# Performance work log

Hardware: AMD Instinct MI355X
Metric: run time of the kernel (lower is better)

## Reference

```python
import jax, jax.numpy as jnp
import numpy as np

NPOINT = 1024
K = 16
D_MODEL = 512
EPS = 1e-5


def _fps(xyz, npoint):
    # deterministic farthest point sampling (start at index 0)
    B, N, _ = xyz.shape
    def step(carry, _):
        dist, far = carry                                   # [B,N], [B]
        cent = jnp.take_along_axis(xyz, far[:, None, None], axis=1)  # [B,1,3]
        d = jnp.sum((xyz - cent) ** 2, axis=-1)             # [B,N]
        dist = jnp.minimum(dist, d)
        nxt = jnp.argmax(dist, axis=-1).astype(jnp.int32)
        return (dist, nxt), far
    init = (jnp.full((B, N), 1e10, xyz.dtype), jnp.zeros((B,), jnp.int32))
    _, idx = jax.lax.scan(step, init, None, length=npoint)
    return jnp.transpose(idx)                                # [B, npoint]


def _bn_relu(x, gamma, beta):
    # BatchNorm (training-mode batch stats, biased var) over all axes but channel-last
    axes = tuple(range(x.ndim - 1))
    mu = jnp.mean(x, axes, keepdims=True)
    var = jnp.var(x, axes, keepdims=True)
    return jax.nn.relu((x - mu) * jax.lax.rsqrt(var + EPS) * gamma + beta)


def _forward(xyz, feat, w1, b1, g1, bt1, fc1_w, fc1_b, wq, wk, wv, fc2_w, fc2_b,
             w2, b2, g2, bt2):
    B, N, C = feat.shape
    fps_idx = _fps(xyz, NPOINT)                              # [B,S]
    new_xyz = jnp.take_along_axis(xyz, fps_idx[:, :, None], axis=1)  # [B,S,3]
    # kNN of sampled centers against all points: squared distances [B,S,N]
    d = (jnp.sum(new_xyz ** 2, -1)[:, :, None]
         + jnp.sum(xyz ** 2, -1)[:, None, :]
         - 2.0 * jnp.einsum('bsc,bnc->bsn', new_xyz, xyz))
    _, knn_idx = jax.lax.top_k(-d, K)                        # [B,S,K]
    grouped = jnp.take_along_axis(
        feat, knn_idx.reshape(B, -1)[:, :, None], axis=1
    ).reshape(B, NPOINT, K, C)                               # [B,S,K,C]
    # mlp1: 1x1 conv + BN + ReLU (channel-last)
    x = _bn_relu(grouped @ w1.T + b1, g1, bt1)
    # TransformerBlock: local self-attention over the K neighbors
    pre = x
    h = x @ fc1_w.T + fc1_b                                  # [B,S,K,D]
    q, kk, v = h @ wq.T, h @ wk.T, h @ wv.T
    attn = jax.nn.softmax(
        jnp.einsum('bsnd,bsmd->bsnm', q, kk) / np.sqrt(D_MODEL), axis=-1)
    res = jnp.einsum('bsnm,bsmd->bsnd', attn, v)
    x = res @ fc2_w.T + fc2_b + pre                          # [B,S,K,C]
    # mlp2: 1x1 conv + BN + ReLU -> out_channel
    x = _bn_relu(x @ w2.T + b2, g2, bt2)                     # [B,S,K,out]
    new_feat = jnp.max(x, axis=2)                            # max-pool over neighbors
    return new_xyz, new_feat


def setup_inputs() -> dict:
    key = jax.random.key(0)
    ks = jax.random.split(key, 12)
    s = 0.02
    return {
        'xyz': jax.random.uniform(ks[0], (8, 4096, 3), jnp.float32),
        'feat': jax.random.normal(ks[1], (8, 4096, 64), jnp.float32),
        'w1': jax.random.normal(ks[2], (64, 64), jnp.float32) * s,
        'b1': jnp.zeros((64,), jnp.float32),
        'g1': jnp.ones((64,), jnp.float32),
        'bt1': jnp.zeros((64,), jnp.float32),
        'fc1_w': jax.random.normal(ks[3], (512, 64), jnp.float32) * s,
        'fc1_b': jnp.zeros((512,), jnp.float32),
        'wq': jax.random.normal(ks[4], (512, 512), jnp.float32) * s,
        'wk': jax.random.normal(ks[5], (512, 512), jnp.float32) * s,
        'wv': jax.random.normal(ks[6], (512, 512), jnp.float32) * s,
        'fc2_w': jax.random.normal(ks[7], (64, 512), jnp.float32) * s,
        'fc2_b': jnp.zeros((64,), jnp.float32),
        'w2': jax.random.normal(ks[8], (128, 64), jnp.float32) * s,
        'b2': jnp.zeros((128,), jnp.float32),
        'g2': jnp.ones((128,), jnp.float32),
        'bt2': jnp.zeros((128,), jnp.float32),
    }


def reference(xyz, feat, w1, b1, g1, bt1, fc1_w, fc1_b, wq, wk, wv, fc2_w, fc2_b,
              w2, b2, g2, bt2):
    return _forward(xyz, feat, w1, b1, g1, bt1, fc1_w, fc1_b, wq, wk, wv,
                    fc2_w, fc2_b, w2, b2, g2, bt2)
```

## Files before the change

kernel.cpp:

```cpp
#include <hip/hip_runtime.h>

#define EPSBN 1e-5f
#define INVSQ 0.04419417382415922f

#define WS_KNN_IDX   32768u
#define WS_X1        1048576u
#define WS_BNP1      34603008u
#define WS_BN1S      34865152u
#define WS_BNP2      34865664u
#define WS_BN2S      35914240u
#define WS_A         35915264u
#define WS_B         36046336u
#define WS_QB        36177408u
#define WS_KB        36179456u
#define WS_WC        36181504u
#define WS_G         36312576u
#define WS_ZT        36328960u
#define WS_U         36345344u
#define WS_W         36345600u
#define WS_TB        36345856u
#define WS_CC        36346112u
#define WS_PTS4      36346368u

__global__ __launch_bounds__(256) void prep1_kernel(const float* __restrict__ wq,
                                                    const float* __restrict__ wk,
                                                    const float* __restrict__ fc1w,
                                                    const float* __restrict__ fc1b,
                                                    const float* __restrict__ fc2w,
                                                    const float* __restrict__ wv,
                                                    const float* __restrict__ xyz,
                                                    float* __restrict__ A, float* __restrict__ B,
                                                    float* __restrict__ qb, float* __restrict__ kb,
                                                    float* __restrict__ Wc,
                                                    float4* __restrict__ pts4) {
  const int blk = blockIdx.x;
  if (blk < 256) {
    int id = blk * 256 + threadIdx.x;
    int which = id >> 15;
    int rem = id & 32767;
    int r = rem >> 6, i = rem & 63;
    const float* W = which ? wk : wq;
    float s = 0.f;
    for (int d = 0; d < 512; ++d) s = fmaf(W[r * 512 + d], fc1w[d * 64 + i], s);
    (which ? B : A)[r * 64 + i] = s;
    if (i == 0) {
      float sb = 0.f;
      for (int d = 0; d < 512; ++d) sb = fmaf(W[r * 512 + d], fc1b[d], sb);
      (which ? kb : qb)[r] = sb;
    }
  } else if (blk < 384) {
    int id = (blk - 256) * 256 + threadIdx.x;
    int c = id >> 9, d = id & 511;
    float s = 0.f;
    for (int e = 0; e < 512; ++e) s = fmaf(fc2w[c * 512 + e], wv[e * 512 + d], s);
    Wc[c * 512 + d] = s;
  } else {
    int id = (blk - 384) * 256 + threadIdx.x;
    float x = xyz[id * 3 + 0], y = xyz[id * 3 + 1], z = xyz[id * 3 + 2];
    float pp = __fadd_rn(__fadd_rn(__fmul_rn(x, x), __fmul_rn(y, y)), __fmul_rn(z, z));
    pts4[id] = make_float4(x, y, z, pp);
  }
}

__global__ __launch_bounds__(256) void prep2_kernel(const float* __restrict__ A,
                                                    const float* __restrict__ B,
                                                    const float* __restrict__ qb,
                                                    const float* __restrict__ kb,
                                                    const float* __restrict__ Wc,
                                                    const float* __restrict__ fc1w,
                                                    const float* __restrict__ fc1b,
                                                    const float* __restrict__ fc2b,
                                                    float* __restrict__ G, float* __restrict__ u,
                                                    float* __restrict__ w, float* __restrict__ cc,
                                                    float* __restrict__ ZT, float* __restrict__ tb) {
  const int blk = blockIdx.x;
  if (blk < 17) {
    int id = blk * 256 + threadIdx.x;
    if (id < 4096) {
      int i = id >> 6, j = id & 63;
      float s = 0.f;
      for (int d = 0; d < 512; ++d) s = fmaf(A[d * 64 + i], B[d * 64 + j], s);
      G[i * 64 + j] = s * INVSQ;
    } else if (id < 4160) {
      int i = id - 4096; float s = 0.f;
      for (int d = 0; d < 512; ++d) s = fmaf(A[d * 64 + i], kb[d], s);
      u[i] = s * INVSQ;
    } else if (id < 4224) {
      int j = id - 4160; float s = 0.f;
      for (int d = 0; d < 512; ++d) s = fmaf(B[d * 64 + j], qb[d], s);
      w[j] = s * INVSQ;
    } else if (id == 4224) {
      float s = 0.f;
      for (int d = 0; d < 512; ++d) s = fmaf(qb[d], kb[d], s);
      cc[0] = s * INVSQ;
    }
  } else {
    int id = (blk - 17) * 256 + threadIdx.x;
    if (id < 4096) {
      int i = id >> 6, c = id & 63;
      float s = 0.f;
      for (int d = 0; d < 512; ++d) s = fmaf(Wc[c * 512 + d], fc1w[d * 64 + i], s);
      ZT[i * 64 + c] = s;
    } else if (id < 4160) {
      int c = id - 4096; float s = 0.f;
      for (int d = 0; d < 512; ++d) s = fmaf(Wc[c * 512 + d], fc1b[d], s);
      tb[c] = s + fc2b[c];
    }
  }
}

#define FPS_REDSTEP(CTRL)                                                              \
  {                                                                                    \
    unsigned lo2 = (unsigned)__builtin_amdgcn_update_dpp(0, (int)klo, CTRL, 0xF, 0xF, true); \
    unsigned hi2 = (unsigned)__builtin_amdgcn_update_dpp(0, (int)khi, CTRL, 0xF, 0xF, true); \
    bool tk = (hi2 > khi) || (hi2 == khi && lo2 > klo);                                \
    khi = tk ? hi2 : khi; klo = tk ? lo2 : klo;                                        \
  }

__global__ __launch_bounds__(256) void fps_kernel(const float4* __restrict__ pts4,
                                                  float* __restrict__ out_xyz) {
  __shared__ float4 spts[4096];
  __shared__ float4 cent4[1024];
  __shared__ unsigned long long red[2][4];
  const int b = blockIdx.x;
  const int t = threadIdx.x;
  const int lane = t & 63, wid = t >> 6;
  const float4* pb = pts4 + (size_t)b * 4096;
  float px[16], py[16], pz[16], pd[16];
#pragma unroll
  for (int i = 0; i < 16; ++i) {
    int j = i * 256 + t;
    float4 p = pb[j];
    spts[j] = p;
    px[i] = p.x; py[i] = p.y; pz[i] = p.z; pd[i] = 1e10f;
  }
  __syncthreads();
  float4 c4 = spts[0];
  for (int it = 0; it < 1024; ++it) {
    if (t == 0) cent4[it] = c4;
    float bv = -1.0f; int bj = 0;
#pragma unroll
    for (int i = 0; i < 16; ++i) {
      float dx = __fsub_rn(px[i], c4.x);
      float dy = __fsub_rn(py[i], c4.y);
      float dz = __fsub_rn(pz[i], c4.z);
      float d = __fadd_rn(__fadd_rn(__fmul_rn(dx, dx), __fmul_rn(dy, dy)), __fmul_rn(dz, dz));
      float nd = fminf(pd[i], d);
      pd[i] = nd;
      bool g = nd > bv;
      bv = g ? nd : bv;
      bj = g ? (i * 256 + t) : bj;
    }
    unsigned klo = 4095u - (unsigned)bj;
    unsigned khi = __float_as_uint(bv);
    FPS_REDSTEP(0x111)
    FPS_REDSTEP(0x112)
    FPS_REDSTEP(0x114)
    FPS_REDSTEP(0x118)
    FPS_REDSTEP(0x142)
    FPS_REDSTEP(0x143)
    unsigned wlo = (unsigned)__builtin_amdgcn_readlane((int)klo, 63);
    unsigned whi = (unsigned)__builtin_amdgcn_readlane((int)khi, 63);
    const int par = it & 1;
    if (lane == 0) red[par][wid] = (((unsigned long long)whi) << 32) | wlo;
    __syncthreads();
    const ulonglong2* r2 = reinterpret_cast<const ulonglong2*>(&red[par][0]);
    ulonglong2 ka = r2[0];
    ulonglong2 kb = r2[1];
    unsigned long long m0 = (ka.x > ka.y) ? ka.x : ka.y;
    unsigned long long m1 = (kb.x > kb.y) ? kb.x : kb.y;
    unsigned long long k0 = (m0 > m1) ? m0 : m1;
    int jw = 4095 - (int)(unsigned)(k0 & 0xFFFFFFFFull);
    c4 = spts[jw];
  }
  __syncthreads();
  for (int o = t; o < 3072; o += 256) {
    int j = o / 3;
    int c = o - 3 * j;
    out_xyz[(size_t)b * 3072 + o] = (&cent4[j].x)[c];
  }
}

__global__ __launch_bounds__(256) void knn_kernel(const float4* __restrict__ pts4,
                                                  const float* __restrict__ new_xyz,
                                                  int* __restrict__ knn_idx) {
  const int t = threadIdx.x & 63;
  const int wave = (blockIdx.x << 2) | (threadIdx.x >> 6);
  const int b = wave >> 10;
  const float4* P = pts4 + (size_t)b * 4096;
  const float cx = new_xyz[(size_t)wave * 3 + 0];
  const float cy = new_xyz[(size_t)wave * 3 + 1];
  const float cz = new_xyz[(size_t)wave * 3 + 2];
  const float cc = __fadd_rn(__fadd_rn(__fmul_rn(cx, cx), __fmul_rn(cy, cy)), __fmul_rn(cz, cz));
  float ldd[16]; int ldi[16];
#pragma unroll
  for (int q = 0; q < 16; ++q) { ldd[q] = 3.4e38f; ldi[q] = 0x7fffffff; }
  for (int i = 0; i < 64; ++i) {
    int j = i * 64 + t;
    float4 p = P[j];
    float dot = __fadd_rn(__fadd_rn(__fmul_rn(cx, p.x), __fmul_rn(cy, p.y)), __fmul_rn(cz, p.z));
    float d = __fsub_rn(__fadd_rn(cc, p.w), __fmul_rn(2.0f, dot));
    if (d < ldd[15] || (d == ldd[15] && j < ldi[15])) {
      float cd = d; int ci = j;
#pragma unroll
      for (int q = 0; q < 16; ++q) {
        bool sw = (cd < ldd[q]) || (cd == ldd[q] && ci < ldi[q]);
        float td = ldd[q]; int ti = ldi[q];
        if (sw) { ldd[q] = cd; ldi[q] = ci; cd = td; ci = ti; }
      }
    }
  }
  float cd = ldd[0]; int ci = ldi[0];
  int* op = knn_idx + (size_t)wave * 16;
#pragma unroll 1
  for (int k = 0; k < 16; ++k) {
    float wd = cd; int wi = ci;
#pragma unroll
    for (int off = 1; off < 64; off <<= 1) {
      float ov = __shfl_xor(wd, off);
      int   oi = __shfl_xor(wi, off);
      bool tk = (ov < wd) || (ov == wd && oi < wi);
      wd = tk ? ov : wd; wi = tk ? oi : wi;
    }
    if (t == 0) op[k] = wi;
    if (wd == cd && wi == ci) {
#pragma unroll
      for (int q = 0; q < 15; ++q) { ldd[q] = ldd[q + 1]; ldi[q] = ldi[q + 1]; }
      ldd[15] = 3.4e38f; ldi[15] = 0x7fffffff;
    }
    cd = ldd[0]; ci = ldi[0];
  }
}

__global__ __launch_bounds__(256) void mlp1_kernel(const float* __restrict__ feat,
                                                   const int* __restrict__ knn_idx,
                                                   const float* __restrict__ w1,
                                                   const float* __restrict__ b1,
                                                   float* __restrict__ x1) {
  __shared__ float w1s[64 * 64];
  __shared__ float b1s[64];
  const int t = threadIdx.x;
  for (int i = t; i < 4096; i += 256) w1s[i] = w1[i];
  if (t < 64) b1s[t] = b1[t];
  __syncthreads();
  const int pos = blockIdx.x * 256 + t;
  const int b = pos >> 14;
  const int n = knn_idx[pos];
  const float4* fp = reinterpret_cast<const float4*>(feat + ((size_t)(b * 4096 + n)) * 64);
  float4 fr[16];
#pragma unroll
  for (int i = 0; i < 16; ++i) fr[i] = fp[i];
  float4* op = reinterpret_cast<float4*>(x1 + (size_t)pos * 64);
#pragma unroll
  for (int cq = 0; cq < 16; ++cq) {
    float a0 = b1s[cq * 4 + 0], a1 = b1s[cq * 4 + 1], a2 = b1s[cq * 4 + 2], a3 = b1s[cq * 4 + 3];
#pragma unroll
    for (int iq = 0; iq < 16; ++iq) {
      float4 f4 = fr[iq];
      float4 wa = *reinterpret_cast<const float4*>(&w1s[(cq * 4 + 0) * 64 + iq * 4]);
      float4 wb = *reinterpret_cast<const float4*>(&w1s[(cq * 4 + 1) * 64 + iq * 4]);
      float4 wc = *reinterpret_cast<const float4*>(&w1s[(cq * 4 + 2) * 64 + iq * 4]);
      float4 wd = *reinterpret_cast<const float4*>(&w1s[(cq * 4 + 3) * 64 + iq * 4]);
      a0 += f4.x * wa.x + f4.y * wa.y + f4.z * wa.z + f4.w * wa.w;
      a1 += f4.x * wb.x + f4.y * wb.y + f4.z * wb.z + f4.w * wb.w;
      a2 += f4.x * wc.x + f4.y * wc.y + f4.z * wc.z + f4.w * wc.w;
      a3 += f4.x * wd.x + f4.y * wd.y + f4.z * wd.z + f4.w * wd.w;
    }
    op[cq] = make_float4(a0, a1, a2, a3);
  }
}

__global__ __launch_bounds__(256) void bn1_stats_kernel(const float* __restrict__ x1,
                                                        float* __restrict__ bnp1) {
  __shared__ float ls[4][64], lq[4][64];
  const int t = threadIdx.x, c = t & 63, g = t >> 6;
  const float* p = x1 + ((size_t)blockIdx.x * 256 + g * 64) * 64 + c;
  float s = 0.f, s2 = 0.f;
  for (int i = 0; i < 64; ++i) { float v = p[(size_t)i * 64]; s += v; s2 = fmaf(v, v, s2); }
  ls[g][c] = s; lq[g][c] = s2;
  __syncthreads();
  if (t < 64) {
    bnp1[blockIdx.x * 128 + t]      = ls[0][t] + ls[1][t] + ls[2][t] + ls[3][t];
    bnp1[blockIdx.x * 128 + 64 + t] = lq[0][t] + lq[1][t] + lq[2][t] + lq[3][t];
  }
}

__global__ __launch_bounds__(256) void bn1_final_kernel(const float* __restrict__ bnp1,
                                                        const float* __restrict__ g1,
                                                        const float* __restrict__ bt1,
                                                        float* __restrict__ bn1s) {
  __shared__ float rs[4][64], rq[4][64];
  const int t = threadIdx.x, c = t & 63, g = t >> 6;
  float S = 0.f, Q = 0.f;
  for (int i = g * 128; i < g * 128 + 128; ++i) {
    S += bnp1[i * 128 + c];
    Q += bnp1[i * 128 + 64 + c];
  }
  rs[g][c] = S; rq[g][c] = Q;
  __syncthreads();
  if (t < 64) {
    float Sa = rs[0][t] + rs[1][t] + rs[2][t] + rs[3][t];
    float Qa = rq[0][t] + rq[1][t] + rq[2][t] + rq[3][t];
    float m = Sa * (1.0f / 131072.0f);
    float var = Qa * (1.0f / 131072.0f) - m * m;
    float sc = g1[t] * rsqrtf(var + EPSBN);
    bn1s[t] = sc;
    bn1s[64 + t] = bt1[t] - m * sc;
  }
}

__global__ __launch_bounds__(64) void transformer_fused(
    float* __restrict__ x1, const float* __restrict__ bn1s,
    const float* __restrict__ G, const float* __restrict__ u, const float* __restrict__ w,
    const float* __restrict__ cc, const float* __restrict__ ZT, const float* __restrict__ tb) {
  __shared__ float pre[16][65];
  __shared__ float ts[16][65];
  __shared__ float ys[16][65];
  __shared__ float ss[16][17];
  __shared__ float spu[16], spw[16];
  const int c = threadIdx.x;
  const size_t base = (size_t)blockIdx.x * 1024;
  const float sc = bn1s[c], sh = bn1s[64 + c];
  float pc[16];
#pragma unroll
  for (int k = 0; k < 16; ++k) {
    float v = x1[base + k * 64 + c];
    float p = fmaxf(0.f, v * sc + sh);
    pc[k] = p; pre[k][c] = p;
  }
  __syncthreads();
  float tcol[16], ycol[16];
#pragma unroll
  for (int k = 0; k < 16; ++k) { tcol[k] = 0.f; ycol[k] = 0.f; }
  for (int i = 0; i < 64; ++i) {
    float g = G[i * 64 + c];
    float z = ZT[i * 64 + c];
#pragma unroll
    for (int k = 0; k < 16; ++k) {
      float p = pre[k][i];
      tcol[k] = fmaf(p, g, tcol[k]);
      ycol[k] = fmaf(p, z, ycol[k]);
    }
  }
#pragma unroll
  for (int k = 0; k < 16; ++k) { ts[k][c] = tcol[k]; ys[k][c] = ycol[k]; }
  if (c < 16) {
    float s = 0.f;
    for (int i = 0; i < 64; ++i) s = fmaf(pre[c][i], u[i], s);
    spu[c] = s;
  } else if (c < 32) {
    int m = c - 16; float s = 0.f;
    for (int i = 0; i < 64; ++i) s = fmaf(pre[m][i], w[i], s);
    spw[m] = s;
  }
  __syncthreads();
  {
    const float cval = cc[0];
    const int m = c & 15, nb = c >> 4;
#pragma unroll
    for (int ng = 0; ng < 4; ++ng) {
      int n = ng * 4 + nb;
      float s = 0.f;
      for (int i = 0; i < 64; ++i) s = fmaf(ts[n][i], pre[m][i], s);
      ss[n][m] = s + spu[n] + spw[m] + cval;
    }
  }
  __syncthreads();
  if (c < 16) {
    float mx = -3.4e38f;
#pragma unroll
    for (int m = 0; m < 16; ++m) mx = fmaxf(mx, ss[c][m]);
    float e[16], sum = 0.f;
#pragma unroll
    for (int m = 0; m < 16; ++m) { e[m] = expf(ss[c][m] - mx); sum += e[m]; }
    float r = 1.0f / sum;
#pragma unroll
    for (int m = 0; m < 16; ++m) ss[c][m] = e[m] * r;
  }
  __syncthreads();
  const float tbc = tb[c];
  float o[16];
#pragma unroll
  for (int k = 0; k < 16; ++k) o[k] = 0.f;
#pragma unroll
  for (int m = 0; m < 16; ++m) {
    float yv = ys[m][c];
#pragma unroll
    for (int k = 0; k < 16; ++k) o[k] = fmaf(ss[k][m], yv, o[k]);
  }
#pragma unroll
  for (int k = 0; k < 16; ++k) x1[base + k * 64 + c] = o[k] + tbc + pc[k];
}

__global__ __launch_bounds__(256) void bn2_stats_kernel(const float* __restrict__ x2,
                                                        const float* __restrict__ w2,
                                                        const float* __restrict__ b2,
                                                        float* __restrict__ bnp2) {
  __shared__ float sx2[128 * 64];
  __shared__ float ps[2][128], pq[2][128];
  const int t = threadIdx.x;
  const float4* s4 = reinterpret_cast<const float4*>(x2 + (size_t)blockIdx.x * 128 * 64);
  float4* d4 = reinterpret_cast<float4*>(sx2);
  for (int i = 0; i < 8; ++i) d4[i * 256 + t] = s4[i * 256 + t];
  __syncthreads();
  const int c = t & 127, h = t >> 7;
  float4 wreg[16];
  const float4* w4 = reinterpret_cast<const float4*>(w2 + c * 64);
#pragma unroll
  for (int i = 0; i < 16; ++i) wreg[i] = w4[i];
  const float bb = b2[c];
  float s = 0.f, q = 0.f;
  for (int p = 0; p < 64; ++p) {
    const float4* xr = reinterpret_cast<const float4*>(&sx2[(h * 64 + p) * 64]);
    float acc = bb;
#pragma unroll
    for (int i = 0; i < 16; ++i) {
      float4 xv = xr[i];
      acc += xv.x * wreg[i].x + xv.y * wreg[i].y + xv.z * wreg[i].z + xv.w * wreg[i].w;
    }
    s += acc; q = fmaf(acc, acc, q);
  }
  ps[h][c] = s; pq[h][c] = q;
  __syncthreads();
  if (t < 128) {
    bnp2[blockIdx.x * 256 + t]       = ps[0][t] + ps[1][t];
    bnp2[blockIdx.x * 256 + 128 + t] = pq[0][t] + pq[1][t];
  }
}

__global__ __launch_bounds__(512) void bn2_final_kernel(const float* __restrict__ bnp2,
                                                        const float* __restrict__ g2,
                                                        const float* __restrict__ bt2,
                                                        float* __restrict__ bn2s) {
  __shared__ float rs[4][128], rq[4][128];
  const int t = threadIdx.x, c = t & 127, g = t >> 7;
  float S = 0.f, Q = 0.f;
  for (int i = g * 256; i < g * 256 + 256; ++i) {
    S += bnp2[i * 256 + c];
    Q += bnp2[i * 256 + 128 + c];
  }
  rs[g][c] = S; rq[g][c] = Q;
  __syncthreads();
  if (t < 128) {
    float Sa = rs[0][t] + rs[1][t] + rs[2][t] + rs[3][t];
    float Qa = rq[0][t] + rq[1][t] + rq[2][t] + rq[3][t];
    float m = Sa * (1.0f / 131072.0f);
    float var = Qa * (1.0f / 131072.0f) - m * m;
    float sc = g2[t] * rsqrtf(var + EPSBN);
    bn2s[t] = sc;
    bn2s[128 + t] = bt2[t] - m * sc;
  }
}

__global__ __launch_bounds__(128) void final_kernel(const float* __restrict__ x2,
                                                    const float* __restrict__ w2,
                                                    const float* __restrict__ b2,
                                                    const float* __restrict__ bn2s,
                                                    float* __restrict__ out) {
  __shared__ float sx2[16 * 64];
  const int t = threadIdx.x;
  const float4* s4 = reinterpret_cast<const float4*>(x2 + (size_t)blockIdx.x * 1024);
  float4* d4 = reinterpret_cast<float4*>(sx2);
  for (int i = 0; i < 2; ++i) d4[i * 128 + t] = s4[i * 128 + t];
  __syncthreads();
  const int c = t;
  float4 wreg[16];
  const float4* w4 = reinterpret_cast<const float4*>(w2 + c * 64);
#pragma unroll
  for (int i = 0; i < 16; ++i) wreg[i] = w4[i];
  const float bb = b2[c], sc = bn2s[c], sh = bn2s[128 + c];
  float mx = -3.4e38f;
  for (int k = 0; k < 16; ++k) {
    const float4* xr = reinterpret_cast<const float4*>(&sx2[k * 64]);
    float acc = bb;
#pragma unroll
    for (int i = 0; i < 16; ++i) {
      float4 xv = xr[i];
      acc += xv.x * wreg[i].x + xv.y * wreg[i].y + xv.z * wreg[i].z + xv.w * wreg[i].w;
    }
    float y = fmaxf(0.f, acc * sc + sh);
    mx = fmaxf(mx, y);
  }
  out[24576 + (size_t)blockIdx.x * 128 + c] = mx;
}

extern "C" void kernel_launch(void* const* d_in, const int* in_sizes, int n_in,
                              void* d_out, int out_size, void* d_ws, size_t ws_size,
                              hipStream_t stream) {
  const float* xyz  = (const float*)d_in[0];
  const float* feat = (const float*)d_in[1];
  const float* w1   = (const float*)d_in[2];
  const float* b1   = (const float*)d_in[3];
  const float* g1   = (const float*)d_in[4];
  const float* bt1  = (const float*)d_in[5];
  const float* fc1w = (const float*)d_in[6];
  const float* fc1b = (const float*)d_in[7];
  const float* wq   = (const float*)d_in[8];
  const float* wk   = (const float*)d_in[9];
  const float* wv   = (const float*)d_in[10];
  const float* fc2w = (const float*)d_in[11];
  const float* fc2b = (const float*)d_in[12];
  const float* w2   = (const float*)d_in[13];
  const float* b2   = (const float*)d_in[14];
  const float* g2   = (const float*)d_in[15];
  const float* bt2  = (const float*)d_in[16];
  float* out = (float*)d_out;
  char* ws = (char*)d_ws;

  int*    knn_idx = (int*)(ws + WS_KNN_IDX);
  float*  x1      = (float*)(ws + WS_X1);
  float*  bnp1    = (float*)(ws + WS_BNP1);
  float*  bn1s    = (float*)(ws + WS_BN1S);
  float*  bnp2    = (float*)(ws + WS_BNP2);
  float*  bn2s    = (float*)(ws + WS_BN2S);
  float*  Abuf    = (float*)(ws + WS_A);
  float*  Bbuf    = (float*)(ws + WS_B);
  float*  qb      = (float*)(ws + WS_QB);
  float*  kb      = (float*)(ws + WS_KB);
  float*  Wc      = (float*)(ws + WS_WC);
  float*  G       = (float*)(ws + WS_G);
  float*  ZT      = (float*)(ws + WS_ZT);
  float*  u       = (float*)(ws + WS_U);
  float*  w       = (float*)(ws + WS_W);
  float*  tb      = (float*)(ws + WS_TB);
  float*  cc      = (float*)(ws + WS_CC);
  float4* pts4    = (float4*)(ws + WS_PTS4);

  prep1_kernel<<<512, 256, 0, stream>>>(wq, wk, fc1w, fc1b, fc2w, wv, xyz,
                                        Abuf, Bbuf, qb, kb, Wc, pts4);
  prep2_kernel<<<34, 256, 0, stream>>>(Abuf, Bbuf, qb, kb, Wc, fc1w, fc1b, fc2b,
                                       G, u, w, cc, ZT, tb);

  fps_kernel<<<8, 256, 0, stream>>>(pts4, out);
  knn_kernel<<<2048, 256, 0, stream>>>(pts4, out, knn_idx);
  mlp1_kernel<<<512, 256, 0, stream>>>(feat, knn_idx, w1, b1, x1);
  bn1_stats_kernel<<<512, 256, 0, stream>>>(x1, bnp1);
  bn1_final_kernel<<<1, 256, 0, stream>>>(bnp1, g1, bt1, bn1s);
  transformer_fused<<<8192, 64, 0, stream>>>(x1, bn1s, G, u, w, cc, ZT, tb);
  bn2_stats_kernel<<<1024, 256, 0, stream>>>(x1, w2, b2, bnp2);
  bn2_final_kernel<<<1, 512, 0, stream>>>(bnp2, g2, bt2, bn2s);
  final_kernel<<<8192, 128, 0, stream>>>(x1, w2, b2, bn2s, out);
}
```

Before: 1.323 ms.

## Fuse prep2 into FPS launch, keep FPS centroids in registers, fuse BN1 stats

Merges the prep2 weight-precompute blocks into the FPS launch as extra blocks so they run alongside the 8 long-running FPS blocks. FPS no longer stages all points in shared memory. Each wave extracts its candidate centroid coordinates from registers with readlane and publishes them next to the reduction key, which removes a dependent LDS lookup on the serial per-iteration path. BN1 partial statistics are computed at the end of mlp1 instead of in a separate kernel, dropping a launch, at the cost of an extra block barrier and re-reading x1 from global memory.

```diff
diff --git a/kernel.cpp b/kernel.cpp
--- a/kernel.cpp
+++ b/kernel.cpp
@@ -62,53 +62,6 @@
   }
 }
 
-__global__ __launch_bounds__(256) void prep2_kernel(const float* __restrict__ A,
-                                                    const float* __restrict__ B,
-                                                    const float* __restrict__ qb,
-                                                    const float* __restrict__ kb,
-                                                    const float* __restrict__ Wc,
-                                                    const float* __restrict__ fc1w,
-                                                    const float* __restrict__ fc1b,
-                                                    const float* __restrict__ fc2b,
-                                                    float* __restrict__ G, float* __restrict__ u,
-                                                    float* __restrict__ w, float* __restrict__ cc,
-                                                    float* __restrict__ ZT, float* __restrict__ tb) {
-  const int blk = blockIdx.x;
-  if (blk < 17) {
-    int id = blk * 256 + threadIdx.x;
-    if (id < 4096) {
-      int i = id >> 6, j = id & 63;
-      float s = 0.f;
-      for (int d = 0; d < 512; ++d) s = fmaf(A[d * 64 + i], B[d * 64 + j], s);
-      G[i * 64 + j] = s * INVSQ;
-    } else if (id < 4160) {
-      int i = id - 4096; float s = 0.f;
-      for (int d = 0; d < 512; ++d) s = fmaf(A[d * 64 + i], kb[d], s);
-      u[i] = s * INVSQ;
-    } else if (id < 4224) {
-      int j = id - 4160; float s = 0.f;
-      for (int d = 0; d < 512; ++d) s = fmaf(B[d * 64 + j], qb[d], s);
-      w[j] = s * INVSQ;
-    } else if (id == 4224) {
-      float s = 0.f;
-      for (int d = 0; d < 512; ++d) s = fmaf(qb[d], kb[d], s);
-      cc[0] = s * INVSQ;
-    }
-  } else {
-    int id = (blk - 17) * 256 + threadIdx.x;
-    if (id < 4096) {
-      int i = id >> 6, c = id & 63;
-      float s = 0.f;
-      for (int d = 0; d < 512; ++d) s = fmaf(Wc[c * 512 + d], fc1w[d * 64 + i], s);
-      ZT[i * 64 + c] = s;
-    } else if (id < 4160) {
-      int c = id - 4096; float s = 0.f;
-      for (int d = 0; d < 512; ++d) s = fmaf(Wc[c * 512 + d], fc1b[d], s);
-      tb[c] = s + fc2b[c];
-    }
-  }
-}
-
 #define FPS_REDSTEP(CTRL)                                                              \
   {                                                                                    \
     unsigned lo2 = (unsigned)__builtin_amdgcn_update_dpp(0, (int)klo, CTRL, 0xF, 0xF, true); \
@@ -117,11 +70,54 @@
     khi = tk ? hi2 : khi; klo = tk ? lo2 : klo;                                        \
   }
 
-__global__ __launch_bounds__(256) void fps_kernel(const float4* __restrict__ pts4,
-                                                  float* __restrict__ out_xyz) {
-  __shared__ float4 spts[4096];
+__global__ __launch_bounds__(256) void fps_prep2_kernel(
+    const float4* __restrict__ pts4, float* __restrict__ out_xyz,
+    const float* __restrict__ A, const float* __restrict__ B,
+    const float* __restrict__ qb, const float* __restrict__ kb,
+    const float* __restrict__ Wc, const float* __restrict__ fc1w,
+    const float* __restrict__ fc1b, const float* __restrict__ fc2b,
+    float* __restrict__ G, float* __restrict__ u, float* __restrict__ w,
+    float* __restrict__ cc, float* __restrict__ ZT, float* __restrict__ tb) {
+  if (blockIdx.x >= 8) {
+    const int blk = blockIdx.x - 8;
+    if (blk < 17) {
+      int id = blk * 256 + threadIdx.x;
+      if (id < 4096) {
+        int i = id >> 6, j = id & 63;
+        float s = 0.f;
+        for (int d = 0; d < 512; ++d) s = fmaf(A[d * 64 + i], B[d * 64 + j], s);
+        G[i * 64 + j] = s * INVSQ;
+      } else if (id < 4160) {
+        int i = id - 4096; float s = 0.f;
+        for (int d = 0; d < 512; ++d) s = fmaf(A[d * 64 + i], kb[d], s);
+        u[i] = s * INVSQ;
+      } else if (id < 4224) {
+        int j = id - 4160; float s = 0.f;
+        for (int d = 0; d < 512; ++d) s = fmaf(B[d * 64 + j], qb[d], s);
+        w[j] = s * INVSQ;
+      } else if (id == 4224) {
+        float s = 0.f;
+        for (int d = 0; d < 512; ++d) s = fmaf(qb[d], kb[d], s);
+        cc[0] = s * INVSQ;
+      }
+    } else {
+      int id = (blk - 17) * 256 + threadIdx.x;
+      if (id < 4096) {
+        int i = id >> 6, c = id & 63;
+        float s = 0.f;
+        for (int d = 0; d < 512; ++d) s = fmaf(Wc[c * 512 + d], fc1w[d * 64 + i], s);
+        ZT[i * 64 + c] = s;
+      } else if (id < 4160) {
+        int c = id - 4096; float s = 0.f;
+        for (int d = 0; d < 512; ++d) s = fmaf(Wc[c * 512 + d], fc1b[d], s);
+        tb[c] = s + fc2b[c];
+      }
+    }
+    return;
+  }
   __shared__ float4 cent4[1024];
-  __shared__ unsigned long long red[2][4];
+  __shared__ unsigned long long redk[2][4];
+  __shared__ float4 redc[2][4];
   const int b = blockIdx.x;
   const int t = threadIdx.x;
   const int lane = t & 63, wid = t >> 6;
@@ -129,21 +125,19 @@
   float px[16], py[16], pz[16], pd[16];
 #pragma unroll
   for (int i = 0; i < 16; ++i) {
-    int j = i * 256 + t;
-    float4 p = pb[j];
-    spts[j] = p;
+    float4 p = pb[i * 256 + t];
     px[i] = p.x; py[i] = p.y; pz[i] = p.z; pd[i] = 1e10f;
   }
-  __syncthreads();
-  float4 c4 = spts[0];
+  float4 cini = pb[0];
+  float cx = cini.x, cy = cini.y, cz = cini.z;
   for (int it = 0; it < 1024; ++it) {
-    if (t == 0) cent4[it] = c4;
+    if (t == 0) cent4[it] = make_float4(cx, cy, cz, 0.f);
     float bv = -1.0f; int bj = 0;
 #pragma unroll
     for (int i = 0; i < 16; ++i) {
-      float dx = __fsub_rn(px[i], c4.x);
-      float dy = __fsub_rn(py[i], c4.y);
-      float dz = __fsub_rn(pz[i], c4.z);
+      float dx = __fsub_rn(px[i], cx);
+      float dy = __fsub_rn(py[i], cy);
+      float dz = __fsub_rn(pz[i], cz);
       float d = __fadd_rn(__fadd_rn(__fmul_rn(dx, dx), __fmul_rn(dy, dy)), __fmul_rn(dz, dz));
       float nd = fminf(pd[i], d);
       pd[i] = nd;
@@ -161,17 +155,48 @@
     FPS_REDSTEP(0x143)
     unsigned wlo = (unsigned)__builtin_amdgcn_readlane((int)klo, 63);
     unsigned whi = (unsigned)__builtin_amdgcn_readlane((int)khi, 63);
+    int jw = 4095 - (int)wlo;
+    int ol = jw & 63;
+    int slot = jw >> 8;
+    float ox, oy, oz;
+    switch (slot) {
+      case 0:  ox = px[0];  oy = py[0];  oz = pz[0];  break;
+      case 1:  ox = px[1];  oy = py[1];  oz = pz[1];  break;
+      case 2:  ox = px[2];  oy = py[2];  oz = pz[2];  break;
+      case 3:  ox = px[3];  oy = py[3];  oz = pz[3];  break;
+      case 4:  ox = px[4];  oy = py[4];  oz = pz[4];  break;
+      case 5:  ox = px[5];  oy = py[5];  oz = pz[5];  break;
+      case 6:  ox = px[6];  oy = py[6];  oz = pz[6];  break;
+      case 7:  ox = px[7];  oy = py[7];  oz = pz[7];  break;
+      case 8:  ox = px[8];  oy = py[8];  oz = pz[8];  break;
+      case 9:  ox = px[9];  oy = py[9];  oz = pz[9];  break;
+      case 10: ox = px[10]; oy = py[10]; oz = pz[10]; break;
+      case 11: ox = px[11]; oy = py[11]; oz = pz[11]; break;
+      case 12: ox = px[12]; oy = py[12]; oz = pz[12]; break;
+      case 13: ox = px[13]; oy = py[13]; oz = pz[13]; break;
+      default: ox = px[14]; oy = py[14]; oz = pz[14];
+               if (slot == 15) { ox = px[15]; oy = py[15]; oz = pz[15]; }
+    }
+    ox = __int_as_float(__builtin_amdgcn_readlane(__float_as_int(ox), ol));
+    oy = __int_as_float(__builtin_amdgcn_readlane(__float_as_int(oy), ol));
+    oz = __int_as_float(__builtin_amdgcn_readlane(__float_as_int(oz), ol));
     const int par = it & 1;
-    if (lane == 0) red[par][wid] = (((unsigned long long)whi) << 32) | wlo;
+    if (lane == 0) {
+      redk[par][wid] = (((unsigned long long)whi) << 32) | wlo;
+      redc[par][wid] = make_float4(ox, oy, oz, 0.f);
+    }
     __syncthreads();
-    const ulonglong2* r2 = reinterpret_cast<const ulonglong2*>(&red[par][0]);
-    ulonglong2 ka = r2[0];
-    ulonglong2 kb = r2[1];
-    unsigned long long m0 = (ka.x > ka.y) ? ka.x : ka.y;
-    unsigned long long m1 = (kb.x > kb.y) ? kb.x : kb.y;
-    unsigned long long k0 = (m0 > m1) ? m0 : m1;
-    int jw = 4095 - (int)(unsigned)(k0 & 0xFFFFFFFFull);
-    c4 = spts[jw];
+    ulonglong2 k01 = *reinterpret_cast<const ulonglong2*>(&redk[par][0]);
+    ulonglong2 k23 = *reinterpret_cast<const ulonglong2*>(&redk[par][2]);
+    float4 r0 = redc[par][0], r1 = redc[par][1], r2 = redc[par][2], r3 = redc[par][3];
+    bool t01 = k01.y > k01.x;
+    unsigned long long ka = t01 ? k01.y : k01.x;
+    float ax = t01 ? r1.x : r0.x, ay = t01 ? r1.y : r0.y, az = t01 ? r1.z : r0.z;
+    bool t23 = k23.y > k23.x;
+    unsigned long long kb2 = t23 ? k23.y : k23.x;
+    float bx = t23 ? r3.x : r2.x, by = t23 ? r3.y : r2.y, bz = t23 ? r3.z : r2.z;
+    bool tf = kb2 > ka;
+    cx = tf ? bx : ax; cy = tf ? by : ay; cz = tf ? bz : az;
   }
   __syncthreads();
   for (int o = t; o < 3072; o += 256) {
@@ -236,9 +261,11 @@
                                                    const int* __restrict__ knn_idx,
                                                    const float* __restrict__ w1,
                                                    const float* __restrict__ b1,
-                                                   float* __restrict__ x1) {
+                                                   float* __restrict__ x1,
+                                                   float* __restrict__ bnp1) {
   __shared__ float w1s[64 * 64];
   __shared__ float b1s[64];
+  __shared__ float ls[4][64], lq[4][64];
   const int t = threadIdx.x;
   for (int i = t; i < 4096; i += 256) w1s[i] = w1[i];
   if (t < 64) b1s[t] = b1[t];
@@ -268,16 +295,15 @@
     }
     op[cq] = make_float4(a0, a1, a2, a3);
   }
-}
-
-__global__ __launch_bounds__(256) void bn1_stats_kernel(const float* __restrict__ x1,
-                                                        float* __restrict__ bnp1) {
-  __shared__ float ls[4][64], lq[4][64];
-  const int t = threadIdx.x, c = t & 63, g = t >> 6;
-  const float* p = x1 + ((size_t)blockIdx.x * 256 + g * 64) * 64 + c;
-  float s = 0.f, s2 = 0.f;
-  for (int i = 0; i < 64; ++i) { float v = p[(size_t)i * 64]; s += v; s2 = fmaf(v, v, s2); }
-  ls[g][c] = s; lq[g][c] = s2;
+  __threadfence_block();
+  __syncthreads();
+  {
+    const int c2 = t & 63, g = t >> 6;
+    const float* p = x1 + ((size_t)blockIdx.x * 256 + g * 64) * 64 + c2;
+    float s = 0.f, s2 = 0.f;
+    for (int i = 0; i < 64; ++i) { float v = p[(size_t)i * 64]; s += v; s2 = fmaf(v, v, s2); }
+    ls[g][c2] = s; lq[g][c2] = s2;
+  }
   __syncthreads();
   if (t < 64) {
     bnp1[blockIdx.x * 128 + t]      = ls[0][t] + ls[1][t] + ls[2][t] + ls[3][t];
@@ -528,13 +554,10 @@
 
   prep1_kernel<<<512, 256, 0, stream>>>(wq, wk, fc1w, fc1b, fc2w, wv, xyz,
                                         Abuf, Bbuf, qb, kb, Wc, pts4);
-  prep2_kernel<<<34, 256, 0, stream>>>(Abuf, Bbuf, qb, kb, Wc, fc1w, fc1b, fc2b,
-                                       G, u, w, cc, ZT, tb);
-
-  fps_kernel<<<8, 256, 0, stream>>>(pts4, out);
+  fps_prep2_kernel<<<42, 256, 0, stream>>>(pts4, out, Abuf, Bbuf, qb, kb, Wc,
+                                           fc1w, fc1b, fc2b, G, u, w, cc, ZT, tb);
   knn_kernel<<<2048, 256, 0, stream>>>(pts4, out, knn_idx);
-  mlp1_kernel<<<512, 256, 0, stream>>>(feat, knn_idx, w1, b1, x1);
-  bn1_stats_kernel<<<512, 256, 0, stream>>>(x1, bnp1);
+  mlp1_kernel<<<512, 256, 0, stream>>>(feat, knn_idx, w1, b1, x1, bnp1);
   bn1_final_kernel<<<1, 256, 0, stream>>>(bnp1, g1, bt1, bn1s);
   transformer_fused<<<8192, 64, 0, stream>>>(x1, bn1s, G, u, w, cc, ZT, tb);
   bn2_stats_kernel<<<1024, 256, 0, stream>>>(x1, w2, b2, bnp2);
```

Result: slower. 1.565 ms (+18.3%).

## Merge prep2 into FPS launch and fuse BN1 stats into mlp1

Applied to the files above, without the earlier changes.

The prep2 weight-folding work now runs as extra blocks inside the FPS kernel launch, so it executes concurrently with the 8 long-running FPS blocks instead of as a separate serialized launch. The BN1 partial-statistics pass is folded into the end of mlp1, with a block fence and barrier so each block re-reads the x1 tile it just wrote, likely from cache. Together these remove two kernel launches and one extra pass over x1. The cost is more shared memory in mlp1 and a larger, branchier FPS kernel.

```diff
diff --git a/kernel.cpp b/kernel.cpp
--- a/kernel.cpp
+++ b/kernel.cpp
@@ -62,53 +62,6 @@
   }
 }
 
-__global__ __launch_bounds__(256) void prep2_kernel(const float* __restrict__ A,
-                                                    const float* __restrict__ B,
-                                                    const float* __restrict__ qb,
-                                                    const float* __restrict__ kb,
-                                                    const float* __restrict__ Wc,
-                                                    const float* __restrict__ fc1w,
-                                                    const float* __restrict__ fc1b,
-                                                    const float* __restrict__ fc2b,
-                                                    float* __restrict__ G, float* __restrict__ u,
-                                                    float* __restrict__ w, float* __restrict__ cc,
-                                                    float* __restrict__ ZT, float* __restrict__ tb) {
-  const int blk = blockIdx.x;
-  if (blk < 17) {
-    int id = blk * 256 + threadIdx.x;
-    if (id < 4096) {
-      int i = id >> 6, j = id & 63;
-      float s = 0.f;
-      for (int d = 0; d < 512; ++d) s = fmaf(A[d * 64 + i], B[d * 64 + j], s);
-      G[i * 64 + j] = s * INVSQ;
-    } else if (id < 4160) {
-      int i = id - 4096; float s = 0.f;
-      for (int d = 0; d < 512; ++d) s = fmaf(A[d * 64 + i], kb[d], s);
-      u[i] = s * INVSQ;
-    } else if (id < 4224) {
-      int j = id - 4160; float s = 0.f;
-      for (int d = 0; d < 512; ++d) s = fmaf(B[d * 64 + j], qb[d], s);
-      w[j] = s * INVSQ;
-    } else if (id == 4224) {
-      float s = 0.f;
-      for (int d = 0; d < 512; ++d) s = fmaf(qb[d], kb[d], s);
-      cc[0] = s * INVSQ;
-    }
-  } else {
-    int id = (blk - 17) * 256 + threadIdx.x;
-    if (id < 4096) {
-      int i = id >> 6, c = id & 63;
-      float s = 0.f;
-      for (int d = 0; d < 512; ++d) s = fmaf(Wc[c * 512 + d], fc1w[d * 64 + i], s);
-      ZT[i * 64 + c] = s;
-    } else if (id < 4160) {
-      int c = id - 4096; float s = 0.f;
-      for (int d = 0; d < 512; ++d) s = fmaf(Wc[c * 512 + d], fc1b[d], s);
-      tb[c] = s + fc2b[c];
-    }
-  }
-}
-
 #define FPS_REDSTEP(CTRL)                                                              \
   {                                                                                    \
     unsigned lo2 = (unsigned)__builtin_amdgcn_update_dpp(0, (int)klo, CTRL, 0xF, 0xF, true); \
@@ -117,8 +70,51 @@
     khi = tk ? hi2 : khi; klo = tk ? lo2 : klo;                                        \
   }
 
-__global__ __launch_bounds__(256) void fps_kernel(const float4* __restrict__ pts4,
-                                                  float* __restrict__ out_xyz) {
+__global__ __launch_bounds__(256) void fps_prep2_kernel(
+    const float4* __restrict__ pts4, float* __restrict__ out_xyz,
+    const float* __restrict__ A, const float* __restrict__ B,
+    const float* __restrict__ qb, const float* __restrict__ kb,
+    const float* __restrict__ Wc, const float* __restrict__ fc1w,
+    const float* __restrict__ fc1b, const float* __restrict__ fc2b,
+    float* __restrict__ G, float* __restrict__ u, float* __restrict__ w,
+    float* __restrict__ cc, float* __restrict__ ZT, float* __restrict__ tb) {
+  if (blockIdx.x >= 8) {
+    const int blk = blockIdx.x - 8;
+    if (blk < 17) {
+      int id = blk * 256 + threadIdx.x;
+      if (id < 4096) {
+        int i = id >> 6, j = id & 63;
+        float s = 0.f;
+        for (int d = 0; d < 512; ++d) s = fmaf(A[d * 64 + i], B[d * 64 + j], s);
+        G[i * 64 + j] = s * INVSQ;
+      } else if (id < 4160) {
+        int i = id - 4096; float s = 0.f;
+        for (int d = 0; d < 512; ++d) s = fmaf(A[d * 64 + i], kb[d], s);
+        u[i] = s * INVSQ;
+      } else if (id < 4224) {
+        int j = id - 4160; float s = 0.f;
+        for (int d = 0; d < 512; ++d) s = fmaf(B[d * 64 + j], qb[d], s);
+        w[j] = s * INVSQ;
+      } else if (id == 4224) {
+        float s = 0.f;
+        for (int d = 0; d < 512; ++d) s = fmaf(qb[d], kb[d], s);
+        cc[0] = s * INVSQ;
+      }
+    } else {
+      int id = (blk - 17) * 256 + threadIdx.x;
+      if (id < 4096) {
+        int i = id >> 6, c = id & 63;
+        float s = 0.f;
+        for (int d = 0; d < 512; ++d) s = fmaf(Wc[c * 512 + d], fc1w[d * 64 + i], s);
+        ZT[i * 64 + c] = s;
+      } else if (id < 4160) {
+        int c = id - 4096; float s = 0.f;
+        for (int d = 0; d < 512; ++d) s = fmaf(Wc[c * 512 + d], fc1b[d], s);
+        tb[c] = s + fc2b[c];
+      }
+    }
+    return;
+  }
   __shared__ float4 spts[4096];
   __shared__ float4 cent4[1024];
   __shared__ unsigned long long red[2][4];
@@ -166,9 +162,9 @@
     __syncthreads();
     const ulonglong2* r2 = reinterpret_cast<const ulonglong2*>(&red[par][0]);
     ulonglong2 ka = r2[0];
-    ulonglong2 kb = r2[1];
+    ulonglong2 kb2 = r2[1];
     unsigned long long m0 = (ka.x > ka.y) ? ka.x : ka.y;
-    unsigned long long m1 = (kb.x > kb.y) ? kb.x : kb.y;
+    unsigned long long m1 = (kb2.x > kb2.y) ? kb2.x : kb2.y;
     unsigned long long k0 = (m0 > m1) ? m0 : m1;
     int jw = 4095 - (int)(unsigned)(k0 & 0xFFFFFFFFull);
     c4 = spts[jw];
@@ -236,9 +232,11 @@
                                                    const int* __restrict__ knn_idx,
                                                    const float* __restrict__ w1,
                                                    const float* __restrict__ b1,
-                                                   float* __restrict__ x1) {
+                                                   float* __restrict__ x1,
+                                                   float* __restrict__ bnp1) {
   __shared__ float w1s[64 * 64];
   __shared__ float b1s[64];
+  __shared__ float ls[4][64], lq[4][64];
   const int t = threadIdx.x;
   for (int i = t; i < 4096; i += 256) w1s[i] = w1[i];
   if (t < 64) b1s[t] = b1[t];
@@ -268,16 +266,15 @@
     }
     op[cq] = make_float4(a0, a1, a2, a3);
   }
-}
-
-__global__ __launch_bounds__(256) void bn1_stats_kernel(const float* __restrict__ x1,
-                                                        float* __restrict__ bnp1) {
-  __shared__ float ls[4][64], lq[4][64];
-  const int t = threadIdx.x, c = t & 63, g = t >> 6;
-  const float* p = x1 + ((size_t)blockIdx.x * 256 + g * 64) * 64 + c;
-  float s = 0.f, s2 = 0.f;
-  for (int i = 0; i < 64; ++i) { float v = p[(size_t)i * 64]; s += v; s2 = fmaf(v, v, s2); }
-  ls[g][c] = s; lq[g][c] = s2;
+  __threadfence_block();
+  __syncthreads();
+  {
+    const int c2 = t & 63, g = t >> 6;
+    const float* p = x1 + ((size_t)blockIdx.x * 256 + g * 64) * 64 + c2;
+    float s = 0.f, s2 = 0.f;
+    for (int i = 0; i < 64; ++i) { float v = p[(size_t)i * 64]; s += v; s2 = fmaf(v, v, s2); }
+    ls[g][c2] = s; lq[g][c2] = s2;
+  }
   __syncthreads();
   if (t < 64) {
     bnp1[blockIdx.x * 128 + t]      = ls[0][t] + ls[1][t] + ls[2][t] + ls[3][t];
@@ -528,13 +525,10 @@
 
   prep1_kernel<<<512, 256, 0, stream>>>(wq, wk, fc1w, fc1b, fc2w, wv, xyz,
                                         Abuf, Bbuf, qb, kb, Wc, pts4);
-  prep2_kernel<<<34, 256, 0, stream>>>(Abuf, Bbuf, qb, kb, Wc, fc1w, fc1b, fc2b,
-                                       G, u, w, cc, ZT, tb);
-
-  fps_kernel<<<8, 256, 0, stream>>>(pts4, out);
+  fps_prep2_kernel<<<42, 256, 0, stream>>>(pts4, out, Abuf, Bbuf, qb, kb, Wc,
+                                           fc1w, fc1b, fc2b, G, u, w, cc, ZT, tb);
   knn_kernel<<<2048, 256, 0, stream>>>(pts4, out, knn_idx);
-  mlp1_kernel<<<512, 256, 0, stream>>>(feat, knn_idx, w1, b1, x1);
-  bn1_stats_kernel<<<512, 256, 0, stream>>>(x1, bnp1);
+  mlp1_kernel<<<512, 256, 0, stream>>>(feat, knn_idx, w1, b1, x1, bnp1);
   bn1_final_kernel<<<1, 256, 0, stream>>>(bnp1, g1, bt1, bn1s);
   transformer_fused<<<8192, 64, 0, stream>>>(x1, bn1s, G, u, w, cc, ZT, tb);
   bn2_stats_kernel<<<1024, 256, 0, stream>>>(x1, w2, b2, bnp2);
```

Result: no change. 1.303 ms (-1.5%).
